# Performance work log

Hardware: AMD Instinct MI355X
Metric: run time of the kernel (lower is better)

## Reference

```python
import jax, jax.numpy as jnp
import numpy as np
from math import ceil

RATIO = 0.5
NUM_GRAPHS = 512
NODES_PER_GRAPH = 1024
N = NUM_GRAPHS * NODES_PER_GRAPH
C = 64
E = 16 * N


def setup_inputs() -> dict:
    key = jax.random.key(0)
    k1, k2 = jax.random.split(key)
    x = jax.random.normal(k1, (N, C), dtype=jnp.float32)
    edge_index = jax.random.randint(k2, (2, E), 0, N, dtype=jnp.int64)
    batch = jnp.repeat(jnp.arange(NUM_GRAPHS, dtype=jnp.int64), NODES_PER_GRAPH)
    return {"x": x, "edge_index": edge_index, "batch": batch,
            "num_graphs": NUM_GRAPHS, "max_num_nodes": NODES_PER_GRAPH}


def reference(x, edge_index, batch, num_graphs, max_num_nodes):
    n = max_num_nodes
    k_sel = ceil(n * RATIO)
    num_nodes = x.shape[0]
    # per-graph: sorted random subset of k_sel local node ids, offset by graph block
    keys = jax.random.split(jax.random.key(42), num_graphs)
    local = jax.vmap(lambda k: jnp.sort(jax.random.permutation(k, n)[:k_sel]))(keys)  # [B, k_sel]
    offsets = jnp.arange(num_graphs, dtype=local.dtype)[:, None] * n
    perm = (local + offsets).reshape(-1)  # [B*k_sel] global node ids, sorted within each graph

    x_sel = x[perm]
    batch_sel = batch[perm]

    # filter_adj: relabel kept nodes 0..K-1, drop edges touching removed nodes
    idx_dtype = edge_index.dtype
    mask = jnp.full((num_nodes,), -1, dtype=idx_dtype)
    mask = mask.at[perm].set(jnp.arange(perm.shape[0], dtype=idx_dtype))
    row = mask[edge_index[0]]
    col = mask[edge_index[1]]
    keep = (row >= 0) & (col >= 0)
    # fixed-shape variant of the dynamic filter: dropped edges marked -1
    new_edge_index = jnp.where(keep[None, :], jnp.stack([row, col]), -1)
    return (x_sel, new_edge_index, batch_sel, perm)
```

## Files before the change

kernel.cpp:

```cpp
#include <hip/hip_runtime.h>

#define NUM_GRAPHS 512
#define NPG        1024
#define KSEL       512
#define NNODES     (NUM_GRAPHS * NPG)
#define CFEAT      64
#define NEDGE      (16 * NNODES)

typedef int   int4v   __attribute__((ext_vector_type(4)));
typedef float float4v __attribute__((ext_vector_type(4)));

__device__ __forceinline__ unsigned rotl32(unsigned v, int d) {
  return (v << d) | (v >> (32 - d));
}

__device__ __forceinline__ void tf2x32(unsigned k0, unsigned k1,
                                       unsigned x0, unsigned x1,
                                       unsigned& o0, unsigned& o1) {
  unsigned ks2 = k0 ^ k1 ^ 0x1BD11BDAu;
  x0 += k0; x1 += k1;
  x0 += x1; x1 = rotl32(x1, 13); x1 ^= x0;
  x0 += x1; x1 = rotl32(x1, 15); x1 ^= x0;
  x0 += x1; x1 = rotl32(x1, 26); x1 ^= x0;
  x0 += x1; x1 = rotl32(x1, 6);  x1 ^= x0;
  x0 += k1; x1 += ks2 + 1u;
  x0 += x1; x1 = rotl32(x1, 17); x1 ^= x0;
  x0 += x1; x1 = rotl32(x1, 29); x1 ^= x0;
  x0 += x1; x1 = rotl32(x1, 16); x1 ^= x0;
  x0 += x1; x1 = rotl32(x1, 24); x1 ^= x0;
  x0 += ks2; x1 += k0 + 2u;
  x0 += x1; x1 = rotl32(x1, 13); x1 ^= x0;
  x0 += x1; x1 = rotl32(x1, 15); x1 ^= x0;
  x0 += x1; x1 = rotl32(x1, 26); x1 ^= x0;
  x0 += x1; x1 = rotl32(x1, 6);  x1 ^= x0;
  x0 += k0; x1 += k1 + 3u;
  x0 += x1; x1 = rotl32(x1, 17); x1 ^= x0;
  x0 += x1; x1 = rotl32(x1, 29); x1 ^= x0;
  x0 += x1; x1 = rotl32(x1, 16); x1 ^= x0;
  x0 += x1; x1 = rotl32(x1, 24); x1 ^= x0;
  x0 += k1; x1 += ks2 + 4u;
  x0 += x1; x1 = rotl32(x1, 13); x1 ^= x0;
  x0 += x1; x1 = rotl32(x1, 15); x1 ^= x0;
  x0 += x1; x1 = rotl32(x1, 26); x1 ^= x0;
  x0 += x1; x1 = rotl32(x1, 6);  x1 ^= x0;
  x0 += ks2; x1 += k0 + 5u;
  o0 = x0; o1 = x1;
}

__global__ __launch_bounds__(512) void select_kernel(
    const float* __restrict__ x, float* __restrict__ out_x,
    float* __restrict__ out_b, float* __restrict__ out_p,
    unsigned short* __restrict__ mask) {
  __shared__ unsigned long long skeys[NPG];
  __shared__ int flags[NPG];
  __shared__ short ids[KSEL];
  __shared__ int ssum[512];

  const int g = blockIdx.x;
  const int tid = threadIdx.x;

  unsigned kg0, kg1, sk0, sk1;
  tf2x32(0u, 42u, 0u, (unsigned)g, kg0, kg1);
  tf2x32(kg0, kg1, 0u, 1u, sk0, sk1);

  for (int i = tid; i < NPG; i += 512) {
    unsigned b1, b2;
    tf2x32(sk0, sk1, 0u, (unsigned)i, b1, b2);
    unsigned key = b1 ^ b2;
    skeys[i] = ((unsigned long long)key << 32) | (unsigned)i;
    flags[i] = 0;
  }
  __syncthreads();

  for (int k = 2; k <= NPG; k <<= 1) {
    for (int j = k >> 1; j > 0; j >>= 1) {
      for (int i = tid; i < NPG; i += 512) {
        int ixj = i ^ j;
        if (ixj > i) {
          unsigned long long a = skeys[i], b = skeys[ixj];
          bool up = ((i & k) == 0);
          if ((a > b) == up) { skeys[i] = b; skeys[ixj] = a; }
        }
      }
      __syncthreads();
    }
  }

  if (tid < KSEL) flags[(int)(skeys[tid] & (unsigned long long)(NPG - 1))] = 1;
  __syncthreads();

  int i2 = tid * 2;
  int f0 = flags[i2], f1 = flags[i2 + 1];
  int local = f0 + f1;
  ssum[tid] = local;
  __syncthreads();
  for (int off = 1; off < 512; off <<= 1) {
    int v = (tid >= off) ? ssum[tid - off] : 0;
    __syncthreads();
    ssum[tid] += v;
    __syncthreads();
  }
  int pos = ssum[tid] - local;

  {
    int i = i2;
    int node = g * NPG + i;
    unsigned short m0 = f0 ? (unsigned short)pos : (unsigned short)0xFFFF;
    if (f0) {
      ids[pos] = (short)i;
      out_b[g * KSEL + pos] = (float)g;
      out_p[g * KSEL + pos] = (float)node;
      pos++;
    }
    int i_1 = i2 + 1;
    unsigned short m1 = f1 ? (unsigned short)pos : (unsigned short)0xFFFF;
    if (f1) {
      ids[pos] = (short)i_1;
      out_b[g * KSEL + pos] = (float)g;
      out_p[g * KSEL + pos] = (float)(node + 1);
    }
    unsigned packed = (unsigned)m0 | ((unsigned)m1 << 16);
    *((unsigned*)(mask + (size_t)g * NPG + i2)) = packed;
  }
  __syncthreads();

  const float4v* xs = (const float4v*)x;
  float4v* xd = (float4v*)out_x;
  for (int t = tid; t < KSEL * 16; t += 512) {
    int r = t >> 4;
    int c = t & 15;
    int id = ids[r];
    float4v v = __builtin_nontemporal_load(&xs[(size_t)(g * NPG + id) * 16 + c]);
    __builtin_nontemporal_store(v, &xd[(size_t)(g * KSEL + r) * 16 + c]);
  }
}

__global__ __launch_bounds__(256) void edge_kernel(
    const int* __restrict__ ei, const unsigned short* __restrict__ mask,
    float* __restrict__ out_e) {
  const int t = blockIdx.x * 256 + threadIdx.x;
  const int base = t * 8;

  int4v s0 = __builtin_nontemporal_load((const int4v*)(ei + base));
  int4v s1 = __builtin_nontemporal_load((const int4v*)(ei + base + 4));
  int4v d0 = __builtin_nontemporal_load((const int4v*)(ei + (size_t)NEDGE + base));
  int4v d1 = __builtin_nontemporal_load((const int4v*)(ei + (size_t)NEDGE + base + 4));

  int src[8] = {s0.x, s0.y, s0.z, s0.w, s1.x, s1.y, s1.z, s1.w};
  int dst[8] = {d0.x, d0.y, d0.z, d0.w, d1.x, d1.y, d1.z, d1.w};

  unsigned short rs[8];
#pragma unroll
  for (int j = 0; j < 8; ++j) {
    rs[j] = __hip_atomic_load(&mask[src[j]], __ATOMIC_RELAXED,
                              __HIP_MEMORY_SCOPE_AGENT);
  }

  unsigned short cs[8];
#pragma unroll
  for (int j = 0; j < 8; ++j) {
    cs[j] = 0xFFFFu;
    if (rs[j] != 0xFFFFu) {
      cs[j] = __hip_atomic_load(&mask[dst[j]], __ATOMIC_RELAXED,
                                __HIP_MEMORY_SCOPE_AGENT);
    }
  }

  float orow[8], ocol[8];
#pragma unroll
  for (int j = 0; j < 8; ++j) {
    bool k = (rs[j] != 0xFFFFu) && (cs[j] != 0xFFFFu);
    orow[j] = k ? (float)(((src[j] & ~1023) >> 1) + (int)rs[j]) : -1.0f;
    ocol[j] = k ? (float)(((dst[j] & ~1023) >> 1) + (int)cs[j]) : -1.0f;
  }

  float4v r0 = {orow[0], orow[1], orow[2], orow[3]};
  float4v r1 = {orow[4], orow[5], orow[6], orow[7]};
  float4v c0 = {ocol[0], ocol[1], ocol[2], ocol[3]};
  float4v c1 = {ocol[4], ocol[5], ocol[6], ocol[7]};
  __builtin_nontemporal_store(r0, (float4v*)(out_e + base));
  __builtin_nontemporal_store(r1, (float4v*)(out_e + base + 4));
  __builtin_nontemporal_store(c0, (float4v*)(out_e + (size_t)NEDGE + base));
  __builtin_nontemporal_store(c1, (float4v*)(out_e + (size_t)NEDGE + base + 4));
}

extern "C" void kernel_launch(void* const* d_in, const int* in_sizes, int n_in,
                              void* d_out, int out_size, void* d_ws, size_t ws_size,
                              hipStream_t stream) {
  const float* x  = (const float*)d_in[0];
  const int*   ei = (const int*)d_in[1];

  float* out   = (float*)d_out;
  float* out_x = out;
  float* out_e = out + (size_t)NUM_GRAPHS * KSEL * CFEAT;
  float* out_b = out_e + 2 * (size_t)NEDGE;
  float* out_p = out_b + (size_t)NUM_GRAPHS * KSEL;

  unsigned short* mask = (unsigned short*)d_ws;

  select_kernel<<<NUM_GRAPHS, 512, 0, stream>>>(x, out_x, out_b, out_p, mask);
  edge_kernel<<<NEDGE / 2048, 256, 0, stream>>>(ei, mask, out_e);
}
```

Baseline: 327.5 us.

## Replace per-node mask with bitset+prefix table in LDS and fuse gather into edge kernel

The select kernel now emits a compact per-graph bitset with prefix counts (128 KB total) plus the selected local ids, instead of a 1 MB ushort relabel mask. A new fused kernel loads the whole table into shared memory and resolves edge endpoints with shifts and popcount, which replaces random global loads. The feature row gather also moves into this kernel, so the select kernel no longer does it. The trade-off is a 128 KB LDS allocation per 1024-thread block, which allows only one block per CU, on a grid of just 256 blocks, so occupancy may limit memory throughput.

```diff
diff --git a/kernel.cpp b/kernel.cpp
--- a/kernel.cpp
+++ b/kernel.cpp
@@ -6,6 +6,7 @@
 #define NNODES     (NUM_GRAPHS * NPG)
 #define CFEAT      64
 #define NEDGE      (16 * NNODES)
+#define NWORDS     (NUM_GRAPHS * 32)
 
 typedef int   int4v   __attribute__((ext_vector_type(4)));
 typedef float float4v __attribute__((ext_vector_type(4)));
@@ -48,9 +49,8 @@
 }
 
 __global__ __launch_bounds__(512) void select_kernel(
-    const float* __restrict__ x, float* __restrict__ out_x,
     float* __restrict__ out_b, float* __restrict__ out_p,
-    unsigned short* __restrict__ mask) {
+    unsigned long long* __restrict__ tab, unsigned short* __restrict__ ids_ws) {
   __shared__ unsigned long long skeys[NPG];
   __shared__ int flags[NPG];
   __shared__ short ids[KSEL];
@@ -105,83 +105,109 @@
   {
     int i = i2;
     int node = g * NPG + i;
-    unsigned short m0 = f0 ? (unsigned short)pos : (unsigned short)0xFFFF;
     if (f0) {
       ids[pos] = (short)i;
       out_b[g * KSEL + pos] = (float)g;
       out_p[g * KSEL + pos] = (float)node;
       pos++;
     }
-    int i_1 = i2 + 1;
-    unsigned short m1 = f1 ? (unsigned short)pos : (unsigned short)0xFFFF;
     if (f1) {
-      ids[pos] = (short)i_1;
+      ids[pos] = (short)(i + 1);
       out_b[g * KSEL + pos] = (float)g;
       out_p[g * KSEL + pos] = (float)(node + 1);
     }
-    unsigned packed = (unsigned)m0 | ((unsigned)m1 << 16);
-    *((unsigned*)(mask + (size_t)g * NPG + i2)) = packed;
-  }
-  __syncthreads();
-
-  const float4v* xs = (const float4v*)x;
-  float4v* xd = (float4v*)out_x;
-  for (int t = tid; t < KSEL * 16; t += 512) {
-    int r = t >> 4;
-    int c = t & 15;
-    int id = ids[r];
-    float4v v = __builtin_nontemporal_load(&xs[(size_t)(g * NPG + id) * 16 + c]);
-    __builtin_nontemporal_store(v, &xd[(size_t)(g * KSEL + r) * 16 + c]);
-  }
-}
-
-__global__ __launch_bounds__(256) void edge_kernel(
-    const int* __restrict__ ei, const unsigned short* __restrict__ mask,
-    float* __restrict__ out_e) {
-  const int t = blockIdx.x * 256 + threadIdx.x;
-  const int base = t * 8;
-
-  int4v s0 = __builtin_nontemporal_load((const int4v*)(ei + base));
-  int4v s1 = __builtin_nontemporal_load((const int4v*)(ei + base + 4));
-  int4v d0 = __builtin_nontemporal_load((const int4v*)(ei + (size_t)NEDGE + base));
-  int4v d1 = __builtin_nontemporal_load((const int4v*)(ei + (size_t)NEDGE + base + 4));
-
-  int src[8] = {s0.x, s0.y, s0.z, s0.w, s1.x, s1.y, s1.z, s1.w};
-  int dst[8] = {d0.x, d0.y, d0.z, d0.w, d1.x, d1.y, d1.z, d1.w};
-
-  unsigned short rs[8];
-#pragma unroll
-  for (int j = 0; j < 8; ++j) {
-    rs[j] = __hip_atomic_load(&mask[src[j]], __ATOMIC_RELAXED,
-                              __HIP_MEMORY_SCOPE_AGENT);
-  }
-
-  unsigned short cs[8];
-#pragma unroll
-  for (int j = 0; j < 8; ++j) {
-    cs[j] = 0xFFFFu;
-    if (rs[j] != 0xFFFFu) {
-      cs[j] = __hip_atomic_load(&mask[dst[j]], __ATOMIC_RELAXED,
-                                __HIP_MEMORY_SCOPE_AGENT);
-    }
-  }
-
-  float orow[8], ocol[8];
-#pragma unroll
-  for (int j = 0; j < 8; ++j) {
-    bool k = (rs[j] != 0xFFFFu) && (cs[j] != 0xFFFFu);
-    orow[j] = k ? (float)(((src[j] & ~1023) >> 1) + (int)rs[j]) : -1.0f;
-    ocol[j] = k ? (float)(((dst[j] & ~1023) >> 1) + (int)cs[j]) : -1.0f;
-  }
-
-  float4v r0 = {orow[0], orow[1], orow[2], orow[3]};
-  float4v r1 = {orow[4], orow[5], orow[6], orow[7]};
-  float4v c0 = {ocol[0], ocol[1], ocol[2], ocol[3]};
-  float4v c1 = {ocol[4], ocol[5], ocol[6], ocol[7]};
-  __builtin_nontemporal_store(r0, (float4v*)(out_e + base));
-  __builtin_nontemporal_store(r1, (float4v*)(out_e + base + 4));
-  __builtin_nontemporal_store(c0, (float4v*)(out_e + (size_t)NEDGE + base));
-  __builtin_nontemporal_store(c1, (float4v*)(out_e + (size_t)NEDGE + base + 4));
+  }
+
+  if (tid < 32) {
+    unsigned w = 0;
+#pragma unroll
+    for (int j = 0; j < 32; ++j) w |= ((unsigned)(flags[tid * 32 + j] & 1)) << j;
+    unsigned base = (tid == 0) ? 0u : (unsigned)ssum[tid * 16 - 1];
+    tab[g * 32 + tid] = (unsigned long long)w |
+                        ((unsigned long long)base << 32);
+  }
+  __syncthreads();
+
+  if (tid < KSEL) ids_ws[g * KSEL + tid] = (unsigned short)ids[tid];
+}
+
+__global__ __launch_bounds__(1024) void fused_kernel(
+    const float* __restrict__ x, const int* __restrict__ ei,
+    const unsigned long long* __restrict__ tab,
+    const unsigned short* __restrict__ ids_ws,
+    float* __restrict__ out_x, float* __restrict__ out_e) {
+  __shared__ unsigned long long ltab[NWORDS];
+  __shared__ unsigned short lids[1024];
+
+  const int tid = threadIdx.x;
+  const int blk = blockIdx.x;
+
+#pragma unroll
+  for (int k = 0; k < NWORDS / 1024; ++k) {
+    ltab[k * 1024 + tid] = tab[k * 1024 + tid];
+  }
+  {
+    const int row0 = blk * 1024;
+    if (tid < 512) {
+      ((unsigned*)lids)[tid] = ((const unsigned*)(ids_ws + row0))[tid];
+    }
+  }
+  __syncthreads();
+
+  {
+    const float4v* xs = (const float4v*)x;
+    float4v* xd = (float4v*)out_x;
+    const int row0 = blk * 1024;
+#pragma unroll
+    for (int k = 0; k < 16; ++k) {
+      int t = k * 1024 + tid;
+      int r = t >> 4;
+      int c = t & 15;
+      int row = row0 + r;
+      int g = row >> 9;
+      int id = lids[r];
+      float4v v = __builtin_nontemporal_load(
+          &xs[((size_t)g * NPG + id) * 16 + c]);
+      __builtin_nontemporal_store(v, &xd[(size_t)row * 16 + c]);
+    }
+  }
+
+#pragma unroll
+  for (int k = 0; k < 4; ++k) {
+    const int base = (((k * 256 + blk) * 1024) + tid) * 8;
+    int4v s0 = __builtin_nontemporal_load((const int4v*)(ei + base));
+    int4v s1 = __builtin_nontemporal_load((const int4v*)(ei + base + 4));
+    int4v d0 = __builtin_nontemporal_load((const int4v*)(ei + (size_t)NEDGE + base));
+    int4v d1 = __builtin_nontemporal_load((const int4v*)(ei + (size_t)NEDGE + base + 4));
+
+    int src[8] = {s0.x, s0.y, s0.z, s0.w, s1.x, s1.y, s1.z, s1.w};
+    int dst[8] = {d0.x, d0.y, d0.z, d0.w, d1.x, d1.y, d1.z, d1.w};
+
+    int rrow[8], rcol[8];
+#pragma unroll
+    for (int j = 0; j < 8; ++j) {
+      unsigned long long es = ltab[src[j] >> 5];
+      unsigned long long ed = ltab[dst[j] >> 5];
+      unsigned ws = (unsigned)es, wd = (unsigned)ed;
+      int shs = src[j] & 31, shd = dst[j] & 31;
+      bool sels = (ws >> shs) & 1u;
+      bool seld = (wd >> shd) & 1u;
+      int poss = (int)(es >> 32) + __popc(ws & ((1u << shs) - 1u));
+      int posd = (int)(ed >> 32) + __popc(wd & ((1u << shd) - 1u));
+      bool keep = sels && seld;
+      rrow[j] = keep ? (((src[j] & ~1023) >> 1) + poss) : -1;
+      rcol[j] = keep ? (((dst[j] & ~1023) >> 1) + posd) : -1;
+    }
+
+    float4v r0 = {(float)rrow[0], (float)rrow[1], (float)rrow[2], (float)rrow[3]};
+    float4v r1 = {(float)rrow[4], (float)rrow[5], (float)rrow[6], (float)rrow[7]};
+    float4v c0 = {(float)rcol[0], (float)rcol[1], (float)rcol[2], (float)rcol[3]};
+    float4v c1 = {(float)rcol[4], (float)rcol[5], (float)rcol[6], (float)rcol[7]};
+    __builtin_nontemporal_store(r0, (float4v*)(out_e + base));
+    __builtin_nontemporal_store(r1, (float4v*)(out_e + base + 4));
+    __builtin_nontemporal_store(c0, (float4v*)(out_e + (size_t)NEDGE + base));
+    __builtin_nontemporal_store(c1, (float4v*)(out_e + (size_t)NEDGE + base + 4));
+  }
 }
 
 extern "C" void kernel_launch(void* const* d_in, const int* in_sizes, int n_in,
@@ -196,8 +222,9 @@
   float* out_b = out_e + 2 * (size_t)NEDGE;
   float* out_p = out_b + (size_t)NUM_GRAPHS * KSEL;
 
-  unsigned short* mask = (unsigned short*)d_ws;
-
-  select_kernel<<<NUM_GRAPHS, 512, 0, stream>>>(x, out_x, out_b, out_p, mask);
-  edge_kernel<<<NEDGE / 2048, 256, 0, stream>>>(ei, mask, out_e);
-}
+  unsigned long long* tab = (unsigned long long*)d_ws;
+  unsigned short* ids_ws = (unsigned short*)((char*)d_ws + NWORDS * 8);
+
+  select_kernel<<<NUM_GRAPHS, 512, 0, stream>>>(out_b, out_p, tab, ids_ws);
+  fused_kernel<<<256, 1024, 0, stream>>>(x, ei, tab, ids_ws, out_x, out_e);
+}
```

After: 301.8 us. -7.8%, faster.
